# Optimization experiments

Measured on AMD Instinct MI355X. Metric: run time of the kernel, lower is better.

## Reference

```python
import jax, jax.numpy as jnp
import numpy as np

B, N, D = 4, 8192, 512
L, W, S = 64, 64, 32  # num_tokens, win_size, stride


def setup_inputs() -> dict:
    key = jax.random.key(0)
    ks = jax.random.split(key, 12)
    inp = {
        "feats": jax.random.normal(ks[0], (B, N, D), jnp.float32),
        "coords": jax.random.normal(ks[1], (B, N, 2), jnp.float32) * 100.0,
        "mask": jnp.zeros((B, N), dtype=bool),
        "z": jax.random.normal(ks[2], (L, D), jnp.float32) * 0.02,
        "Wq": jax.random.normal(ks[3], (D, D), jnp.float32) * 0.01,
        "Wk": jax.random.normal(ks[4], (D, D), jnp.float32) * 0.01,
        "Wv": jax.random.normal(ks[5], (D, D), jnp.float32) * 0.01,
        "W1": jax.random.normal(ks[6], (D, 2), jnp.float32) * 0.05,
        "b1": jnp.zeros((D,), jnp.float32),
        "W2": jax.random.normal(ks[7], (D, D), jnp.float32) * 0.01,
        "b2": jnp.zeros((D,), jnp.float32),
        "Wo": jax.random.normal(ks[8], (D, D), jnp.float32) * 0.01,
        "bo": jnp.zeros((D,), jnp.float32),
    }
    return inp


def reference(feats, coords, mask, z, Wq, Wk, Wv, W1, b1, W2, b2, Wo, bo):
    # mask is all-False: every token valid, N_valid == N, segments are
    # contiguous blocks of P = N // L tokens (seg_id = floor(i*L/N)).
    Bz, Nn, Dd = feats.shape
    Ll = z.shape[0]
    P = Nn // Ll  # tokens per segment

    # LayerNorm over feature dim (no affine, eps=1e-5 as in F.layer_norm)
    mu = feats.mean(-1, keepdims=True)
    var = feats.var(-1, keepdims=True)
    f_ln = (feats - mu) * jax.lax.rsqrt(var + 1e-5)

    # per-sample coordinate normalization (torch std is unbiased, ddof=1)
    c_mu = coords.mean(1, keepdims=True)
    c_sd = coords.std(1, keepdims=True, ddof=1) + 1e-8
    c_n = (coords - c_mu) / c_sd

    f_seg = f_ln.reshape(Bz, Ll, P, Dd)
    c_seg = c_n.reshape(Bz, Ll, P, 2)

    # static sliding windows within each segment (last window may be partial)
    starts = np.arange(0, P, S)                      # [nw]
    idx = starts[:, None] + np.arange(W)[None, :]    # [nw, W]
    valid = jnp.asarray(idx < P)                     # [nw, W] bool
    idx_c = np.minimum(idx, P - 1)
    cnt = valid.sum(-1).astype(feats.dtype)          # [nw]

    f_win = f_seg[:, :, idx_c]                       # [B,L,nw,W,D]
    c_win = c_seg[:, :, idx_c]                       # [B,L,nw,W,2]

    vmask = valid.astype(feats.dtype)[None, None, :, :, None]
    c_mean = (c_win * vmask).sum(3) / cnt[None, None, :, None]   # [B,L,nw,2]
    pos_in = c_win - c_mean[:, :, :, None, :]
    h = jax.nn.relu(jnp.einsum('blnwc,dc->blnwd', pos_in, W1) + b1)
    pos_bias = jnp.einsum('blnwd,ed->blnwe', h, W2) + b2

    q = z @ Wq.T                                     # [L,D]
    k = jnp.einsum('blnwd,ed->blnwe', f_win, Wk) + pos_bias
    v = jnp.einsum('blnwd,ed->blnwe', f_win, Wv)

    temperature = jnp.sqrt(jnp.asarray(Dd, feats.dtype))
    logits = jnp.einsum('ld,blnwd->blnw', q, k) / temperature
    logits = jnp.clip(logits, -10.0, 10.0)
    logits = jnp.where(valid[None, None], logits, -jnp.inf)
    attn = jax.nn.softmax(logits, axis=-1)           # [B,L,nw,W]

    z_win = jnp.einsum('blnw,blnwd->blnd', attn, v)  # [B,L,nw,D]
    z_l = z_win.mean(2)                              # average over windows
    return z_l @ Wo.T + bo                           # [B,L,D]
```

## Files before the change

kernel.cpp:

```cpp
#include <hip/hip_runtime.h>

#define Bz 4
#define Nn 8192
#define Dd 512
#define Ll 64
#define Pp 128
#define Ww 64
#define Ss 32
#define NW 4

__global__ __launch_bounds__(256) void pre1(
    const float* __restrict__ coords, const float* __restrict__ b2,
    const float* __restrict__ Wq, const float* __restrict__ Wk,
    const float* __restrict__ W2,
    const float* __restrict__ Wv, const float* __restrict__ Wo,
    float* __restrict__ cstats,
    float* __restrict__ M1, float* __restrict__ M2,
    float* __restrict__ WvoT, float* __restrict__ vb8) {
    __shared__ float As[64][68];
    __shared__ float Bs[64][68];
    __shared__ float b2s[64];
    __shared__ double dred[16];
    int bid = blockIdx.x, tid = threadIdx.x;
    int wv = tid >> 6, lane = tid & 63;

    if (bid < 192) {
        int role = bid >> 6;
        int wb = bid & 63;
        int m0 = (wb >> 3) * 64;
        int n0 = (wb & 7) * 64;
        const float* Amat = (role == 2) ? Wv : Wq;
        const float* Bmat = (role == 0) ? Wk : (role == 1) ? W2 : Wo;
        float* Cmat = (role == 0) ? M1 : (role == 1) ? M2 : WvoT;
        int tx = tid & 15, ty = tid >> 4;
        float4 acc[4];
#pragma unroll
        for (int i = 0; i < 4; ++i) acc[i] = make_float4(0.f, 0.f, 0.f, 0.f);

        for (int k0 = 0; k0 < Dd; k0 += 64) {
            {
                int kk = tid >> 4, q4 = (tid & 15) * 4;
#pragma unroll
                for (int i = 0; i < 4; ++i) {
                    int k = kk + 16 * i;
                    *(float4*)&As[k][q4] =
                        *(const float4*)&Amat[(size_t)(k0 + k) * Dd + m0 + q4];
                }
                if (role != 2) {
#pragma unroll
                    for (int i = 0; i < 4; ++i) {
                        int k = kk + 16 * i;
                        *(float4*)&Bs[k][q4] =
                            *(const float4*)&Bmat[(size_t)(k0 + k) * Dd + n0 + q4];
                    }
                } else {
                    int d = tid >> 2;
#pragma unroll
                    for (int j = 0; j < 4; ++j) {
                        int c0 = (tid & 3) * 16 + 4 * j;
                        float4 v = *(const float4*)&Bmat[(size_t)(n0 + d) * Dd + k0 + c0];
                        Bs[c0 + 0][d] = v.x; Bs[c0 + 1][d] = v.y;
                        Bs[c0 + 2][d] = v.z; Bs[c0 + 3][d] = v.w;
                    }
                }
            }
            __syncthreads();
#pragma unroll 8
            for (int kk = 0; kk < 64; ++kk) {
                float4 a4 = *(const float4*)&As[kk][ty * 4];
                float4 b4 = *(const float4*)&Bs[kk][tx * 4];
                acc[0].x = fmaf(a4.x, b4.x, acc[0].x); acc[0].y = fmaf(a4.x, b4.y, acc[0].y);
                acc[0].z = fmaf(a4.x, b4.z, acc[0].z); acc[0].w = fmaf(a4.x, b4.w, acc[0].w);
                acc[1].x = fmaf(a4.y, b4.x, acc[1].x); acc[1].y = fmaf(a4.y, b4.y, acc[1].y);
                acc[1].z = fmaf(a4.y, b4.z, acc[1].z); acc[1].w = fmaf(a4.y, b4.w, acc[1].w);
                acc[2].x = fmaf(a4.z, b4.x, acc[2].x); acc[2].y = fmaf(a4.z, b4.y, acc[2].y);
                acc[2].z = fmaf(a4.z, b4.z, acc[2].z); acc[2].w = fmaf(a4.z, b4.w, acc[2].w);
                acc[3].x = fmaf(a4.w, b4.x, acc[3].x); acc[3].y = fmaf(a4.w, b4.y, acc[3].y);
                acc[3].z = fmaf(a4.w, b4.z, acc[3].z); acc[3].w = fmaf(a4.w, b4.w, acc[3].w);
            }
            __syncthreads();
        }
#pragma unroll
        for (int i = 0; i < 4; ++i)
            *(float4*)&Cmat[(size_t)(m0 + ty * 4 + i) * Dd + n0 + tx * 4] = acc[i];
    } else if (bid < 200) {
        int j = bid - 192;
        if (tid < 64) b2s[tid] = b2[j * 64 + tid];
        __syncthreads();
        float a0 = 0.f, a1 = 0.f;
#pragma unroll 4
        for (int ee = 0; ee < 64; ++ee) {
            int e = j * 64 + ee;
            float be = b2s[ee];
            a0 = fmaf(be, Wq[(size_t)e * Dd + tid], a0);
            a1 = fmaf(be, Wq[(size_t)e * Dd + tid + 256], a1);
        }
        vb8[j * Dd + tid] = a0;
        vb8[j * Dd + tid + 256] = a1;
    } else {
        int b = bid - 200;
        double sx = 0, sy = 0, sxx = 0, syy = 0;
        const float4* cp = (const float4*)(coords + (size_t)b * Nn * 2);
        for (int i = tid; i < Nn / 2; i += 256) {
            float4 v = cp[i];
            sx  += (double)v.x + (double)v.z;
            sy  += (double)v.y + (double)v.w;
            sxx += (double)v.x * v.x + (double)v.z * v.z;
            syy += (double)v.y * v.y + (double)v.w * v.w;
        }
        for (int o = 32; o > 0; o >>= 1) {
            sx  += __shfl_down(sx,  o); sy  += __shfl_down(sy,  o);
            sxx += __shfl_down(sxx, o); syy += __shfl_down(syy, o);
        }
        if (lane == 0) {
            dred[wv * 4 + 0] = sx;  dred[wv * 4 + 1] = sy;
            dred[wv * 4 + 2] = sxx; dred[wv * 4 + 3] = syy;
        }
        __syncthreads();
        if (tid == 0) {
            double tx = 0, ty = 0, txx = 0, tyy = 0;
            for (int i = 0; i < 4; ++i) {
                tx += dred[i * 4 + 0]; ty += dred[i * 4 + 1];
                txx += dred[i * 4 + 2]; tyy += dred[i * 4 + 3];
            }
            const double N = (double)Nn;
            double mux = tx / N, muy = ty / N;
            double vx = (txx - N * mux * mux) / (N - 1.0);
            double vy = (tyy - N * muy * muy) / (N - 1.0);
            cstats[b * 4 + 0] = (float)mux;
            cstats[b * 4 + 1] = (float)muy;
            cstats[b * 4 + 2] = (float)sqrt(vx) + 1e-8f;
            cstats[b * 4 + 3] = (float)sqrt(vy) + 1e-8f;
        }
    }
}

__global__ __launch_bounds__(256) void qkg_k(
    const float* __restrict__ z, const float* __restrict__ M1,
    const float* __restrict__ M2, const float* __restrict__ vb8,
    float* __restrict__ QK, float* __restrict__ G,
    float* __restrict__ sqk4, float* __restrict__ qb2) {
    __shared__ float zs[Dd];
    __shared__ float pq[8][128];
    __shared__ float pg[8][128];
    __shared__ float red[8];
    int bid = blockIdx.x, tid = threadIdx.x;
    int l = bid & 63, ch = bid >> 6;
    int wv = tid >> 6, lane = tid & 63;

    zs[tid]       = z[(size_t)l * Dd + tid];
    zs[tid + 256] = z[(size_t)l * Dd + tid + 256];
    __syncthreads();

    if (ch == 0) {
        float vba = 0.f, vbb = 0.f;
#pragma unroll
        for (int j = 0; j < 8; ++j) {
            vba += vb8[j * Dd + tid];
            vbb += vb8[j * Dd + tid + 256];
        }
        float p = zs[tid] * vba + zs[tid + 256] * vbb;
        for (int o = 32; o > 0; o >>= 1) p += __shfl_xor(p, o);
        if (lane == 0) red[4 + wv] = p;
    }

    {
        int qd = tid & 31, h = tid >> 5;
        int cb = ch * 128 + qd * 4;
        float4 aq = make_float4(0.f, 0.f, 0.f, 0.f);
        float4 ag = make_float4(0.f, 0.f, 0.f, 0.f);
        for (int d = h * 64; d < h * 64 + 64; ++d) {
            float zd = zs[d];
            float4 m1 = *(const float4*)&M1[(size_t)d * Dd + cb];
            float4 m2 = *(const float4*)&M2[(size_t)d * Dd + cb];
            aq.x = fmaf(zd, m1.x, aq.x); aq.y = fmaf(zd, m1.y, aq.y);
            aq.z = fmaf(zd, m1.z, aq.z); aq.w = fmaf(zd, m1.w, aq.w);
            ag.x = fmaf(zd, m2.x, ag.x); ag.y = fmaf(zd, m2.y, ag.y);
            ag.z = fmaf(zd, m2.z, ag.z); ag.w = fmaf(zd, m2.w, ag.w);
        }
        *(float4*)&pq[h][qd * 4] = aq;
        *(float4*)&pg[h][qd * 4] = ag;
    }
    __syncthreads();
    if (tid < 128) {
        float vq = 0.f, vg = 0.f;
#pragma unroll
        for (int hh = 0; hh < 8; ++hh) { vq += pq[hh][tid]; vg += pg[hh][tid]; }
        QK[(size_t)l * Dd + ch * 128 + tid] = vq;
        G [(size_t)l * Dd + ch * 128 + tid] = vg;
        float s = vq;
        for (int o = 32; o > 0; o >>= 1) s += __shfl_xor(s, o);
        if (lane == 0) red[wv] = s;
    }
    __syncthreads();
    if (tid == 0) sqk4[ch * 64 + l] = red[0] + red[1];
    if (ch == 0 && tid == 32) qb2[l] = red[4] + red[5] + red[6] + red[7];
}

__global__ __launch_bounds__(1024) void attn2(
    const float* __restrict__ feats, const float* __restrict__ coords,
    const float* __restrict__ cstats,
    const float* __restrict__ QKm, const float* __restrict__ Gm,
    const float* __restrict__ sqk4, const float* __restrict__ qb2,
    const float* __restrict__ W1, const float* __restrict__ b1,
    const float* __restrict__ WvoT, const float* __restrict__ bo,
    float* __restrict__ out) {
    __shared__ float  qk_s[Dd];
    __shared__ float4 wpack[Dd];
    __shared__ float  scx[Pp], scy[Pp];
    __shared__ float  smu[Pp], srs[Pp], sa[Pp];
    __shared__ float  shs[NW * Ww];
    __shared__ float  sar[NW][Ww];
    __shared__ float  swt[Pp];
    __shared__ float  s2red[NW];
    __shared__ float  soff;
    __shared__ float  red16[16][Dd];

    int bx = blockIdx.x;
    int l = bx & 63, b = bx >> 6;
    int tid = threadIdx.x;
    int wv = tid >> 6, lane = tid & 63;

    if (tid < Dd) {
        qk_s[tid] = QKm[l * Dd + tid];
    } else {
        int t = tid - Dd;
        wpack[t] = make_float4(W1[2 * t], W1[2 * t + 1], b1[t], Gm[l * Dd + t]);
    }
    if (tid < Pp) {
        int row = bx * Pp + tid;
        float x = coords[(size_t)row * 2], y = coords[(size_t)row * 2 + 1];
        scx[tid] = (x - cstats[b * 4 + 0]) / cstats[b * 4 + 2];
        scy[tid] = (y - cstats[b * 4 + 1]) / cstats[b * 4 + 3];
    }
    float sqk_l = sqk4[l] + sqk4[64 + l] + sqk4[128 + l] + sqk4[192 + l];
    float qb2_l = qb2[l];
    __syncthreads();

    const float* fbase = feats + (size_t)bx * Pp * Dd;
    int rb = wv * 8;
    float4 f0[8], f1[8];
#pragma unroll
    for (int i = 0; i < 8; ++i) {
        const float4* fr = (const float4*)(fbase + (size_t)(rb + i) * Dd);
        f0[i] = fr[lane];
        f1[i] = fr[lane + 64];
    }
    __builtin_amdgcn_sched_barrier(0);

    float cmx[4], cmy[4];
#pragma unroll
    for (int n = 0; n < 4; ++n) {
        int nv = (n == 3) ? 32 : 64;
        float cx = (lane < nv) ? scx[n * Ss + lane] : 0.f;
        float cy = (lane < nv) ? scy[n * Ss + lane] : 0.f;
        for (int o = 32; o > 0; o >>= 1) { cx += __shfl_xor(cx, o); cy += __shfl_xor(cy, o); }
        cmx[n] = cx / (float)nv; cmy[n] = cy / (float)nv;
    }

    {
        int s = tid >> 2, q = tid & 3;
        int n = s >> 6, w = s & 63;
        int nv = (n == 3) ? 32 : 64;
        float hs = 0.f;
        if (w < nv) {
            int p = n * Ss + w;
            float px = scx[p] - cmx[n], py = scy[p] - cmy[n];
            int d0 = q * 128;
#pragma unroll 4
            for (int d = d0; d < d0 + 128; ++d) {
                float4 c = wpack[d];
                hs = fmaf(c.w, fmaxf(fmaf(c.x, px, fmaf(c.y, py, c.z)), 0.f), hs);
            }
        }
        hs += __shfl_xor(hs, 1);
        hs += __shfl_xor(hs, 2);
        if (q == 0) shs[s] = hs;
    }

    {
        float4 q0 = ((const float4*)qk_s)[lane];
        float4 q1 = ((const float4*)qk_s)[lane + 64];
#pragma unroll
        for (int b2i = 0; b2i < 8; b2i += 4) {
            float sP[4], ssP[4], aP[4];
#pragma unroll
            for (int i = 0; i < 4; ++i) {
                float4 v0 = f0[b2i + i], v1 = f1[b2i + i];
                sP[i]  = v0.x + v0.y + v0.z + v0.w + v1.x + v1.y + v1.z + v1.w;
                ssP[i] = v0.x * v0.x + v0.y * v0.y + v0.z * v0.z + v0.w * v0.w
                       + v1.x * v1.x + v1.y * v1.y + v1.z * v1.z + v1.w * v1.w;
                aP[i]  = v0.x * q0.x + v0.y * q0.y + v0.z * q0.z + v0.w * q0.w
                       + v1.x * q1.x + v1.y * q1.y + v1.z * q1.z + v1.w * q1.w;
            }
#pragma unroll
            for (int o = 32; o > 0; o >>= 1) {
#pragma unroll
                for (int i = 0; i < 4; ++i) {
                    sP[i] += __shfl_xor(sP[i], o); ssP[i] += __shfl_xor(ssP[i], o);
                    aP[i] += __shfl_xor(aP[i], o);
                }
            }
            if (lane == 0) {
#pragma unroll
                for (int i = 0; i < 4; ++i) {
                    int r = rb + b2i + i;
                    float mu  = sP[i] * (1.f / (float)Dd);
                    float var = ssP[i] * (1.f / (float)Dd) - mu * mu;
                    smu[r] = mu; srs[r] = 1.f / sqrtf(var + 1e-5f); sa[r] = aP[i];
                }
            }
        }
    }
    __syncthreads();

    const float invtemp = 0.04419417382415922f;
    if (wv < 4) {
        int n = wv, w = lane;
        int nv = (n == 3) ? 32 : 64;
        int p = n * Ss + ((w < nv) ? w : 0);
        float lg = -1e30f;
        if (w < nv) {
            lg = (srs[p] * (sa[p] - smu[p] * sqk_l) + shs[n * Ww + w] + qb2_l) * invtemp;
            lg = fminf(fmaxf(lg, -10.f), 10.f);
        }
        float m = lg;
        for (int o = 32; o > 0; o >>= 1) m = fmaxf(m, __shfl_xor(m, o));
        float e = (w < nv) ? expf(lg - m) : 0.f;
        float ssum = e;
        for (int o = 32; o > 0; o >>= 1) ssum += __shfl_xor(ssum, o);
        float ar = (w < nv) ? (e / ssum) * srs[p] : 0.f;
        sar[n][w] = ar;
        float t2 = (w < nv) ? ar * smu[p] : 0.f;
        for (int o = 32; o > 0; o >>= 1) t2 += __shfl_xor(t2, o);
        if (lane == 0) s2red[n] = t2;
    }
    __syncthreads();

    if (tid < Pp) {
        int p = tid;
        int na = (p >> 5) - 1, nb = (p >> 5);
        float wt = 0.f;
        if (na >= 0 && na <= 3) wt += sar[na][p - na * Ss];
        if (nb <= 3)            wt += sar[nb][p - nb * Ss];
        swt[p] = wt;
    }
    if (tid == 0) soff = 0.25f * (s2red[0] + s2red[1] + s2red[2] + s2red[3]);
    __syncthreads();

    {
        float4 a0 = make_float4(0.f, 0.f, 0.f, 0.f);
        float4 a1 = make_float4(0.f, 0.f, 0.f, 0.f);
#pragma unroll
        for (int i = 0; i < 8; ++i) {
            float wt = swt[rb + i];
            a0.x = fmaf(wt, f0[i].x, a0.x); a0.y = fmaf(wt, f0[i].y, a0.y);
            a0.z = fmaf(wt, f0[i].z, a0.z); a0.w = fmaf(wt, f0[i].w, a0.w);
            a1.x = fmaf(wt, f1[i].x, a1.x); a1.y = fmaf(wt, f1[i].y, a1.y);
            a1.z = fmaf(wt, f1[i].z, a1.z); a1.w = fmaf(wt, f1[i].w, a1.w);
        }
        *(float4*)&red16[wv][lane * 4]       = a0;
        *(float4*)&red16[wv][256 + lane * 4] = a1;
    }
    __syncthreads();
    if (tid < Dd) {
        float v = 0.f;
#pragma unroll
        for (int w = 0; w < 16; ++w) v += red16[w][tid];
        qk_s[tid] = 0.25f * v - soff;
    }
    __syncthreads();

    {
        int h = tid >> 7, cq = (tid & 127) * 4;
        float4 acc = make_float4(0.f, 0.f, 0.f, 0.f);
#pragma unroll 4
        for (int e = h * 64; e < h * 64 + 64; ++e) {
            float fe = qk_s[e];
            float4 w = *(const float4*)&WvoT[(size_t)e * Dd + cq];
            acc.x = fmaf(fe, w.x, acc.x);
            acc.y = fmaf(fe, w.y, acc.y);
            acc.z = fmaf(fe, w.z, acc.z);
            acc.w = fmaf(fe, w.w, acc.w);
        }
        *(float4*)&red16[h][cq] = acc;
    }
    __syncthreads();
    if (tid < Dd) {
        out[(size_t)bx * Dd + tid] = bo[tid]
            + red16[0][tid] + red16[1][tid] + red16[2][tid] + red16[3][tid]
            + red16[4][tid] + red16[5][tid] + red16[6][tid] + red16[7][tid];
    }
}

extern "C" void kernel_launch(void* const* d_in, const int* in_sizes, int n_in,
                              void* d_out, int out_size, void* d_ws, size_t ws_size,
                              hipStream_t stream) {
    const float* feats  = (const float*)d_in[0];
    const float* coords = (const float*)d_in[1];
    const float* z  = (const float*)d_in[3];
    const float* Wq = (const float*)d_in[4];
    const float* Wk = (const float*)d_in[5];
    const float* Wv = (const float*)d_in[6];
    const float* W1 = (const float*)d_in[7];
    const float* b1 = (const float*)d_in[8];
    const float* W2 = (const float*)d_in[9];
    const float* b2 = (const float*)d_in[10];
    const float* Wo = (const float*)d_in[11];
    const float* bo = (const float*)d_in[12];
    float* out = (float*)d_out;

    float* ws = (float*)d_ws;
    float* cstats = ws;
    float* M1     = ws + 16;
    float* M2     = M1 + Dd * Dd;
    float* WvoT   = M2 + Dd * Dd;
    float* vb8    = WvoT + Dd * Dd;
    float* QK     = vb8 + 8 * Dd;
    float* G      = QK + Ll * Dd;
    float* sqk4   = G + Ll * Dd;
    float* qb2    = sqk4 + 256;

    pre1<<<204, 256, 0, stream>>>(coords, b2, Wq, Wk, W2, Wv, Wo,
                                  cstats, M1, M2, WvoT, vb8);
    qkg_k<<<256, 256, 0, stream>>>(z, M1, M2, vb8, QK, G, sqk4, qb2);
    attn2<<<Bz * Ll, 1024, 0, stream>>>(feats, coords, cstats,
                                        QK, G, sqk4, qb2, W1, b1,
                                        WvoT, bo, out);
}
```

Measured before the change: 174.6 us.

## Fuse three kernels into one cooperative kernel with grid syncs

Replaces the three separate launches (weight-product precompute, per-token query projections, and attention/output) with a single cooperative kernel of 256 blocks by 1024 threads, separated by grid-wide syncs. The aim is to remove launch overhead and inter-kernel gaps between the small stages. In exchange, the first two stages now run on 1024-thread blocks in which only 256 threads are active, and grid.sync adds its own barrier cost.

```diff
diff --git a/kernel.cpp b/kernel.cpp
--- a/kernel.cpp
+++ b/kernel.cpp
@@ -1,4 +1,6 @@
 #include <hip/hip_runtime.h>
+#include <hip/hip_cooperative_groups.h>
+namespace cg = cooperative_groups;
 
 #define Bz 4
 #define Nn 8192
@@ -9,387 +11,396 @@
 #define Ss 32
 #define NW 4
 
-__global__ __launch_bounds__(256) void pre1(
-    const float* __restrict__ coords, const float* __restrict__ b2,
-    const float* __restrict__ Wq, const float* __restrict__ Wk,
-    const float* __restrict__ W2,
-    const float* __restrict__ Wv, const float* __restrict__ Wo,
-    float* __restrict__ cstats,
-    float* __restrict__ M1, float* __restrict__ M2,
-    float* __restrict__ WvoT, float* __restrict__ vb8) {
-    __shared__ float As[64][68];
-    __shared__ float Bs[64][68];
-    __shared__ float b2s[64];
-    __shared__ double dred[16];
+__global__ __launch_bounds__(1024) void fused(
+    const float* __restrict__ feats, const float* __restrict__ coords,
+    const float* __restrict__ z,  const float* __restrict__ Wq,
+    const float* __restrict__ Wk, const float* __restrict__ W2,
+    const float* __restrict__ b2, const float* __restrict__ Wv,
+    const float* __restrict__ Wo, const float* __restrict__ W1,
+    const float* __restrict__ b1, const float* __restrict__ bo,
+    float* cstats, float* M1, float* M2, float* WvoT, float* vb8,
+    float* QK, float* G, float* sqk4, float* qb2, float* out) {
+    cg::grid_group grid = cg::this_grid();
+    __shared__ __align__(16) char smem[48256];
     int bid = blockIdx.x, tid = threadIdx.x;
-    int wv = tid >> 6, lane = tid & 63;
-
-    if (bid < 192) {
-        int role = bid >> 6;
-        int wb = bid & 63;
-        int m0 = (wb >> 3) * 64;
-        int n0 = (wb & 7) * 64;
-        const float* Amat = (role == 2) ? Wv : Wq;
-        const float* Bmat = (role == 0) ? Wk : (role == 1) ? W2 : Wo;
-        float* Cmat = (role == 0) ? M1 : (role == 1) ? M2 : WvoT;
-        int tx = tid & 15, ty = tid >> 4;
-        float4 acc[4];
-#pragma unroll
-        for (int i = 0; i < 4; ++i) acc[i] = make_float4(0.f, 0.f, 0.f, 0.f);
-
-        for (int k0 = 0; k0 < Dd; k0 += 64) {
-            {
-                int kk = tid >> 4, q4 = (tid & 15) * 4;
-#pragma unroll
-                for (int i = 0; i < 4; ++i) {
-                    int k = kk + 16 * i;
-                    *(float4*)&As[k][q4] =
-                        *(const float4*)&Amat[(size_t)(k0 + k) * Dd + m0 + q4];
-                }
-                if (role != 2) {
+
+    {
+        bool act = (tid < 256);
+        int wv4 = tid >> 6, lane = tid & 63;
+        if (bid < 192) {
+            float (*As)[68] = (float (*)[68])smem;
+            float (*Bs)[68] = (float (*)[68])(smem + 17408);
+            int role = bid >> 6;
+            int wb = bid & 63;
+            int m0 = (wb >> 3) * 64;
+            int n0 = (wb & 7) * 64;
+            const float* Amat = (role == 2) ? Wv : Wq;
+            const float* Bmat = (role == 0) ? Wk : (role == 1) ? W2 : Wo;
+            float* Cmat = (role == 0) ? M1 : (role == 1) ? M2 : WvoT;
+            int tx = tid & 15, ty = (tid & 255) >> 4;
+            float4 acc[4];
+#pragma unroll
+            for (int i = 0; i < 4; ++i) acc[i] = make_float4(0.f, 0.f, 0.f, 0.f);
+
+            for (int k0 = 0; k0 < Dd; k0 += 64) {
+                if (act) {
+                    int kk = tid >> 4, q4 = (tid & 15) * 4;
 #pragma unroll
                     for (int i = 0; i < 4; ++i) {
                         int k = kk + 16 * i;
-                        *(float4*)&Bs[k][q4] =
-                            *(const float4*)&Bmat[(size_t)(k0 + k) * Dd + n0 + q4];
+                        *(float4*)&As[k][q4] =
+                            *(const float4*)&Amat[(size_t)(k0 + k) * Dd + m0 + q4];
                     }
-                } else {
-                    int d = tid >> 2;
-#pragma unroll
-                    for (int j = 0; j < 4; ++j) {
-                        int c0 = (tid & 3) * 16 + 4 * j;
-                        float4 v = *(const float4*)&Bmat[(size_t)(n0 + d) * Dd + k0 + c0];
-                        Bs[c0 + 0][d] = v.x; Bs[c0 + 1][d] = v.y;
-                        Bs[c0 + 2][d] = v.z; Bs[c0 + 3][d] = v.w;
+                    if (role != 2) {
+#pragma unroll
+                        for (int i = 0; i < 4; ++i) {
+                            int k = kk + 16 * i;
+                            *(float4*)&Bs[k][q4] =
+                                *(const float4*)&Bmat[(size_t)(k0 + k) * Dd + n0 + q4];
+                        }
+                    } else {
+                        int d = tid >> 2;
+#pragma unroll
+                        for (int j = 0; j < 4; ++j) {
+                            int c0 = (tid & 3) * 16 + 4 * j;
+                            float4 v = *(const float4*)&Bmat[(size_t)(n0 + d) * Dd + k0 + c0];
+                            Bs[c0 + 0][d] = v.x; Bs[c0 + 1][d] = v.y;
+                            Bs[c0 + 2][d] = v.z; Bs[c0 + 3][d] = v.w;
+                        }
                     }
                 }
-            }
+                __syncthreads();
+                if (act) {
+#pragma unroll 8
+                    for (int kk = 0; kk < 64; ++kk) {
+                        float4 a4 = *(const float4*)&As[kk][ty * 4];
+                        float4 b4 = *(const float4*)&Bs[kk][tx * 4];
+                        acc[0].x = fmaf(a4.x, b4.x, acc[0].x); acc[0].y = fmaf(a4.x, b4.y, acc[0].y);
+                        acc[0].z = fmaf(a4.x, b4.z, acc[0].z); acc[0].w = fmaf(a4.x, b4.w, acc[0].w);
+                        acc[1].x = fmaf(a4.y, b4.x, acc[1].x); acc[1].y = fmaf(a4.y, b4.y, acc[1].y);
+                        acc[1].z = fmaf(a4.y, b4.z, acc[1].z); acc[1].w = fmaf(a4.y, b4.w, acc[1].w);
+                        acc[2].x = fmaf(a4.z, b4.x, acc[2].x); acc[2].y = fmaf(a4.z, b4.y, acc[2].y);
+                        acc[2].z = fmaf(a4.z, b4.z, acc[2].z); acc[2].w = fmaf(a4.z, b4.w, acc[2].w);
+                        acc[3].x = fmaf(a4.w, b4.x, acc[3].x); acc[3].y = fmaf(a4.w, b4.y, acc[3].y);
+                        acc[3].z = fmaf(a4.w, b4.z, acc[3].z); acc[3].w = fmaf(a4.w, b4.w, acc[3].w);
+                    }
+                }
+                __syncthreads();
+            }
+            if (act) {
+#pragma unroll
+                for (int i = 0; i < 4; ++i)
+                    *(float4*)&Cmat[(size_t)(m0 + ty * 4 + i) * Dd + n0 + tx * 4] = acc[i];
+            }
+        } else if (bid < 200) {
+            float* b2s = (float*)(smem + 34816);
+            int j = bid - 192;
+            if (act && tid < 64) b2s[tid] = b2[j * 64 + tid];
             __syncthreads();
-#pragma unroll 8
-            for (int kk = 0; kk < 64; ++kk) {
-                float4 a4 = *(const float4*)&As[kk][ty * 4];
-                float4 b4 = *(const float4*)&Bs[kk][tx * 4];
-                acc[0].x = fmaf(a4.x, b4.x, acc[0].x); acc[0].y = fmaf(a4.x, b4.y, acc[0].y);
-                acc[0].z = fmaf(a4.x, b4.z, acc[0].z); acc[0].w = fmaf(a4.x, b4.w, acc[0].w);
-                acc[1].x = fmaf(a4.y, b4.x, acc[1].x); acc[1].y = fmaf(a4.y, b4.y, acc[1].y);
-                acc[1].z = fmaf(a4.y, b4.z, acc[1].z); acc[1].w = fmaf(a4.y, b4.w, acc[1].w);
-                acc[2].x = fmaf(a4.z, b4.x, acc[2].x); acc[2].y = fmaf(a4.z, b4.y, acc[2].y);
-                acc[2].z = fmaf(a4.z, b4.z, acc[2].z); acc[2].w = fmaf(a4.z, b4.w, acc[2].w);
-                acc[3].x = fmaf(a4.w, b4.x, acc[3].x); acc[3].y = fmaf(a4.w, b4.y, acc[3].y);
-                acc[3].z = fmaf(a4.w, b4.z, acc[3].z); acc[3].w = fmaf(a4.w, b4.w, acc[3].w);
+            if (act) {
+                float a0 = 0.f, a1 = 0.f;
+#pragma unroll 4
+                for (int ee = 0; ee < 64; ++ee) {
+                    int e = j * 64 + ee;
+                    float be = b2s[ee];
+                    a0 = fmaf(be, Wq[(size_t)e * Dd + tid], a0);
+                    a1 = fmaf(be, Wq[(size_t)e * Dd + tid + 256], a1);
+                }
+                vb8[j * Dd + tid] = a0;
+                vb8[j * Dd + tid + 256] = a1;
+            }
+        } else if (bid < 204) {
+            double* dred = (double*)(smem + 35072);
+            int b = bid - 200;
+            if (act) {
+                double sx = 0, sy = 0, sxx = 0, syy = 0;
+                const float4* cp = (const float4*)(coords + (size_t)b * Nn * 2);
+                for (int i = tid; i < Nn / 2; i += 256) {
+                    float4 v = cp[i];
+                    sx  += (double)v.x + (double)v.z;
+                    sy  += (double)v.y + (double)v.w;
+                    sxx += (double)v.x * v.x + (double)v.z * v.z;
+                    syy += (double)v.y * v.y + (double)v.w * v.w;
+                }
+                for (int o = 32; o > 0; o >>= 1) {
+                    sx  += __shfl_down(sx,  o); sy  += __shfl_down(sy,  o);
+                    sxx += __shfl_down(sxx, o); syy += __shfl_down(syy, o);
+                }
+                if (lane == 0) {
+                    dred[wv4 * 4 + 0] = sx;  dred[wv4 * 4 + 1] = sy;
+                    dred[wv4 * 4 + 2] = sxx; dred[wv4 * 4 + 3] = syy;
+                }
             }
             __syncthreads();
-        }
-#pragma unroll
-        for (int i = 0; i < 4; ++i)
-            *(float4*)&Cmat[(size_t)(m0 + ty * 4 + i) * Dd + n0 + tx * 4] = acc[i];
-    } else if (bid < 200) {
-        int j = bid - 192;
-        if (tid < 64) b2s[tid] = b2[j * 64 + tid];
-        __syncthreads();
-        float a0 = 0.f, a1 = 0.f;
+            if (tid == 0) {
+                double tx = 0, ty = 0, txx = 0, tyy = 0;
+                for (int i = 0; i < 4; ++i) {
+                    tx += dred[i * 4 + 0]; ty += dred[i * 4 + 1];
+                    txx += dred[i * 4 + 2]; tyy += dred[i * 4 + 3];
+                }
+                const double N = (double)Nn;
+                double mux = tx / N, muy = ty / N;
+                double vx = (txx - N * mux * mux) / (N - 1.0);
+                double vy = (tyy - N * muy * muy) / (N - 1.0);
+                cstats[b * 4 + 0] = (float)mux;
+                cstats[b * 4 + 1] = (float)muy;
+                cstats[b * 4 + 2] = (float)sqrt(vx) + 1e-8f;
+                cstats[b * 4 + 3] = (float)sqrt(vy) + 1e-8f;
+            }
+        }
+    }
+    __threadfence();
+    grid.sync();
+
+    {
+        float* zs        = (float*)smem;
+        float (*pq)[128] = (float (*)[128])(smem + 2048);
+        float (*pg)[128] = (float (*)[128])(smem + 6144);
+        float* redB      = (float*)(smem + 10240);
+        bool act = (tid < 256);
+        int l = bid & 63, ch = bid >> 6;
+        int wv4 = tid >> 6, lane = tid & 63;
+
+        if (act) {
+            zs[tid]       = z[(size_t)l * Dd + tid];
+            zs[tid + 256] = z[(size_t)l * Dd + tid + 256];
+        }
+        __syncthreads();
+        if (act) {
+            if (ch == 0) {
+                float vba = 0.f, vbb = 0.f;
+#pragma unroll
+                for (int j = 0; j < 8; ++j) {
+                    vba += vb8[j * Dd + tid];
+                    vbb += vb8[j * Dd + tid + 256];
+                }
+                float p = zs[tid] * vba + zs[tid + 256] * vbb;
+                for (int o = 32; o > 0; o >>= 1) p += __shfl_xor(p, o);
+                if (lane == 0) redB[4 + wv4] = p;
+            }
+            int qd = tid & 31, h = tid >> 5;
+            int cb = ch * 128 + qd * 4;
+            float4 aq = make_float4(0.f, 0.f, 0.f, 0.f);
+            float4 ag = make_float4(0.f, 0.f, 0.f, 0.f);
+            for (int d = h * 64; d < h * 64 + 64; ++d) {
+                float zd = zs[d];
+                float4 m1 = *(const float4*)&M1[(size_t)d * Dd + cb];
+                float4 m2 = *(const float4*)&M2[(size_t)d * Dd + cb];
+                aq.x = fmaf(zd, m1.x, aq.x); aq.y = fmaf(zd, m1.y, aq.y);
+                aq.z = fmaf(zd, m1.z, aq.z); aq.w = fmaf(zd, m1.w, aq.w);
+                ag.x = fmaf(zd, m2.x, ag.x); ag.y = fmaf(zd, m2.y, ag.y);
+                ag.z = fmaf(zd, m2.z, ag.z); ag.w = fmaf(zd, m2.w, ag.w);
+            }
+            *(float4*)&pq[h][qd * 4] = aq;
+            *(float4*)&pg[h][qd * 4] = ag;
+        }
+        __syncthreads();
+        if (act && tid < 128) {
+            float vq = 0.f, vg = 0.f;
+#pragma unroll
+            for (int hh = 0; hh < 8; ++hh) { vq += pq[hh][tid]; vg += pg[hh][tid]; }
+            QK[(size_t)l * Dd + ch * 128 + tid] = vq;
+            G [(size_t)l * Dd + ch * 128 + tid] = vg;
+            float s = vq;
+            for (int o = 32; o > 0; o >>= 1) s += __shfl_xor(s, o);
+            if (lane == 0) redB[wv4] = s;
+        }
+        __syncthreads();
+        if (tid == 0) sqk4[ch * 64 + l] = redB[0] + redB[1];
+        if (ch == 0 && tid == 32) qb2[l] = redB[4] + redB[5] + redB[6] + redB[7];
+    }
+    __threadfence();
+    grid.sync();
+
+    {
+        float*  qk_s  = (float*)smem;
+        float4* wpack = (float4*)(smem + 2048);
+        float*  scx   = (float*)(smem + 10240);
+        float*  scy   = (float*)(smem + 10752);
+        float*  smu   = (float*)(smem + 11264);
+        float*  srs   = (float*)(smem + 11776);
+        float*  sa    = (float*)(smem + 12288);
+        float*  shs   = (float*)(smem + 12800);
+        float (*sar)[Ww] = (float (*)[Ww])(smem + 13824);
+        float*  swt   = (float*)(smem + 14848);
+        float*  s2red = (float*)(smem + 15360);
+        float*  soff  = (float*)(smem + 15376);
+        float (*red16)[Dd] = (float (*)[Dd])(smem + 15392);
+
+        int bx = bid;
+        int l = bx & 63, b = bx >> 6;
+        int wv = tid >> 6, lane = tid & 63;
+
+        if (tid < Dd) {
+            qk_s[tid] = QK[l * Dd + tid];
+        } else {
+            int t = tid - Dd;
+            wpack[t] = make_float4(W1[2 * t], W1[2 * t + 1], b1[t], G[l * Dd + t]);
+        }
+        if (tid < Pp) {
+            int row = bx * Pp + tid;
+            float x = coords[(size_t)row * 2], y = coords[(size_t)row * 2 + 1];
+            scx[tid] = (x - cstats[b * 4 + 0]) / cstats[b * 4 + 2];
+            scy[tid] = (y - cstats[b * 4 + 1]) / cstats[b * 4 + 3];
+        }
+        float sqk_l = sqk4[l] + sqk4[64 + l] + sqk4[128 + l] + sqk4[192 + l];
+        float qb2_l = qb2[l];
+        __syncthreads();
+
+        const float* fbase = feats + (size_t)bx * Pp * Dd;
+        int rb = wv * 8;
+        float4 f0[8], f1[8];
+#pragma unroll
+        for (int i = 0; i < 8; ++i) {
+            const float4* fr = (const float4*)(fbase + (size_t)(rb + i) * Dd);
+            f0[i] = fr[lane];
+            f1[i] = fr[lane + 64];
+        }
+        __builtin_amdgcn_sched_barrier(0);
+
+        float cmx[4], cmy[4];
+#pragma unroll
+        for (int n = 0; n < 4; ++n) {
+            int nv = (n == 3) ? 32 : 64;
+            float cx = (lane < nv) ? scx[n * Ss + lane] : 0.f;
+            float cy = (lane < nv) ? scy[n * Ss + lane] : 0.f;
+            for (int o = 32; o > 0; o >>= 1) { cx += __shfl_xor(cx, o); cy += __shfl_xor(cy, o); }
+            cmx[n] = cx / (float)nv; cmy[n] = cy / (float)nv;
+        }
+
+        {
+            int s = tid >> 2, q = tid & 3;
+            int n = s >> 6, w = s & 63;
+            int nv = (n == 3) ? 32 : 64;
+            float hs = 0.f;
+            if (w < nv) {
+                int p = n * Ss + w;
+                float px = scx[p] - cmx[n], py = scy[p] - cmy[n];
+                int d0 = q * 128;
 #pragma unroll 4
-        for (int ee = 0; ee < 64; ++ee) {
-            int e = j * 64 + ee;
-            float be = b2s[ee];
-            a0 = fmaf(be, Wq[(size_t)e * Dd + tid], a0);
-            a1 = fmaf(be, Wq[(size_t)e * Dd + tid + 256], a1);
-        }
-        vb8[j * Dd + tid] = a0;
-        vb8[j * Dd + tid + 256] = a1;
-    } else {
-        int b = bid - 200;
-        double sx = 0, sy = 0, sxx = 0, syy = 0;
-        const float4* cp = (const float4*)(coords + (size_t)b * Nn * 2);
-        for (int i = tid; i < Nn / 2; i += 256) {
-            float4 v = cp[i];
-            sx  += (double)v.x + (double)v.z;
-            sy  += (double)v.y + (double)v.w;
-            sxx += (double)v.x * v.x + (double)v.z * v.z;
-            syy += (double)v.y * v.y + (double)v.w * v.w;
-        }
-        for (int o = 32; o > 0; o >>= 1) {
-            sx  += __shfl_down(sx,  o); sy  += __shfl_down(sy,  o);
-            sxx += __shfl_down(sxx, o); syy += __shfl_down(syy, o);
-        }
-        if (lane == 0) {
-            dred[wv * 4 + 0] = sx;  dred[wv * 4 + 1] = sy;
-            dred[wv * 4 + 2] = sxx; dred[wv * 4 + 3] = syy;
-        }
-        __syncthreads();
-        if (tid == 0) {
-            double tx = 0, ty = 0, txx = 0, tyy = 0;
-            for (int i = 0; i < 4; ++i) {
-                tx += dred[i * 4 + 0]; ty += dred[i * 4 + 1];
-                txx += dred[i * 4 + 2]; tyy += dred[i * 4 + 3];
-            }
-            const double N = (double)Nn;
-            double mux = tx / N, muy = ty / N;
-            double vx = (txx - N * mux * mux) / (N - 1.0);
-            double vy = (tyy - N * muy * muy) / (N - 1.0);
-            cstats[b * 4 + 0] = (float)mux;
-            cstats[b * 4 + 1] = (float)muy;
-            cstats[b * 4 + 2] = (float)sqrt(vx) + 1e-8f;
-            cstats[b * 4 + 3] = (float)sqrt(vy) + 1e-8f;
-        }
-    }
-}
-
-__global__ __launch_bounds__(256) void qkg_k(
-    const float* __restrict__ z, const float* __restrict__ M1,
-    const float* __restrict__ M2, const float* __restrict__ vb8,
-    float* __restrict__ QK, float* __restrict__ G,
-    float* __restrict__ sqk4, float* __restrict__ qb2) {
-    __shared__ float zs[Dd];
-    __shared__ float pq[8][128];
-    __shared__ float pg[8][128];
-    __shared__ float red[8];
-    int bid = blockIdx.x, tid = threadIdx.x;
-    int l = bid & 63, ch = bid >> 6;
-    int wv = tid >> 6, lane = tid & 63;
-
-    zs[tid]       = z[(size_t)l * Dd + tid];
-    zs[tid + 256] = z[(size_t)l * Dd + tid + 256];
-    __syncthreads();
-
-    if (ch == 0) {
-        float vba = 0.f, vbb = 0.f;
-#pragma unroll
-        for (int j = 0; j < 8; ++j) {
-            vba += vb8[j * Dd + tid];
-            vbb += vb8[j * Dd + tid + 256];
-        }
-        float p = zs[tid] * vba + zs[tid + 256] * vbb;
-        for (int o = 32; o > 0; o >>= 1) p += __shfl_xor(p, o);
-        if (lane == 0) red[4 + wv] = p;
-    }
-
-    {
-        int qd = tid & 31, h = tid >> 5;
-        int cb = ch * 128 + qd * 4;
-        float4 aq = make_float4(0.f, 0.f, 0.f, 0.f);
-        float4 ag = make_float4(0.f, 0.f, 0.f, 0.f);
-        for (int d = h * 64; d < h * 64 + 64; ++d) {
-            float zd = zs[d];
-            float4 m1 = *(const float4*)&M1[(size_t)d * Dd + cb];
-            float4 m2 = *(const float4*)&M2[(size_t)d * Dd + cb];
-            aq.x = fmaf(zd, m1.x, aq.x); aq.y = fmaf(zd, m1.y, aq.y);
-            aq.z = fmaf(zd, m1.z, aq.z); aq.w = fmaf(zd, m1.w, aq.w);
-            ag.x = fmaf(zd, m2.x, ag.x); ag.y = fmaf(zd, m2.y, ag.y);
-            ag.z = fmaf(zd, m2.z, ag.z); ag.w = fmaf(zd, m2.w, ag.w);
-        }
-        *(float4*)&pq[h][qd * 4] = aq;
-        *(float4*)&pg[h][qd * 4] = ag;
-    }
-    __syncthreads();
-    if (tid < 128) {
-        float vq = 0.f, vg = 0.f;
-#pragma unroll
-        for (int hh = 0; hh < 8; ++hh) { vq += pq[hh][tid]; vg += pg[hh][tid]; }
-        QK[(size_t)l * Dd + ch * 128 + tid] = vq;
-        G [(size_t)l * Dd + ch * 128 + tid] = vg;
-        float s = vq;
-        for (int o = 32; o > 0; o >>= 1) s += __shfl_xor(s, o);
-        if (lane == 0) red[wv] = s;
-    }
-    __syncthreads();
-    if (tid == 0) sqk4[ch * 64 + l] = red[0] + red[1];
-    if (ch == 0 && tid == 32) qb2[l] = red[4] + red[5] + red[6] + red[7];
-}
-
-__global__ __launch_bounds__(1024) void attn2(
-    const float* __restrict__ feats, const float* __restrict__ coords,
-    const float* __restrict__ cstats,
-    const float* __restrict__ QKm, const float* __restrict__ Gm,
-    const float* __restrict__ sqk4, const float* __restrict__ qb2,
-    const float* __restrict__ W1, const float* __restrict__ b1,
-    const float* __restrict__ WvoT, const float* __restrict__ bo,
-    float* __restrict__ out) {
-    __shared__ float  qk_s[Dd];
-    __shared__ float4 wpack[Dd];
-    __shared__ float  scx[Pp], scy[Pp];
-    __shared__ float  smu[Pp], srs[Pp], sa[Pp];
-    __shared__ float  shs[NW * Ww];
-    __shared__ float  sar[NW][Ww];
-    __shared__ float  swt[Pp];
-    __shared__ float  s2red[NW];
-    __shared__ float  soff;
-    __shared__ float  red16[16][Dd];
-
-    int bx = blockIdx.x;
-    int l = bx & 63, b = bx >> 6;
-    int tid = threadIdx.x;
-    int wv = tid >> 6, lane = tid & 63;
-
-    if (tid < Dd) {
-        qk_s[tid] = QKm[l * Dd + tid];
-    } else {
-        int t = tid - Dd;
-        wpack[t] = make_float4(W1[2 * t], W1[2 * t + 1], b1[t], Gm[l * Dd + t]);
-    }
-    if (tid < Pp) {
-        int row = bx * Pp + tid;
-        float x = coords[(size_t)row * 2], y = coords[(size_t)row * 2 + 1];
-        scx[tid] = (x - cstats[b * 4 + 0]) / cstats[b * 4 + 2];
-        scy[tid] = (y - cstats[b * 4 + 1]) / cstats[b * 4 + 3];
-    }
-    float sqk_l = sqk4[l] + sqk4[64 + l] + sqk4[128 + l] + sqk4[192 + l];
-    float qb2_l = qb2[l];
-    __syncthreads();
-
-    const float* fbase = feats + (size_t)bx * Pp * Dd;
-    int rb = wv * 8;
-    float4 f0[8], f1[8];
-#pragma unroll
-    for (int i = 0; i < 8; ++i) {
-        const float4* fr = (const float4*)(fbase + (size_t)(rb + i) * Dd);
-        f0[i] = fr[lane];
-        f1[i] = fr[lane + 64];
-    }
-    __builtin_amdgcn_sched_barrier(0);
-
-    float cmx[4], cmy[4];
-#pragma unroll
-    for (int n = 0; n < 4; ++n) {
-        int nv = (n == 3) ? 32 : 64;
-        float cx = (lane < nv) ? scx[n * Ss + lane] : 0.f;
-        float cy = (lane < nv) ? scy[n * Ss + lane] : 0.f;
-        for (int o = 32; o > 0; o >>= 1) { cx += __shfl_xor(cx, o); cy += __shfl_xor(cy, o); }
-        cmx[n] = cx / (float)nv; cmy[n] = cy / (float)nv;
-    }
-
-    {
-        int s = tid >> 2, q = tid & 3;
-        int n = s >> 6, w = s & 63;
-        int nv = (n == 3) ? 32 : 64;
-        float hs = 0.f;
-        if (w < nv) {
-            int p = n * Ss + w;
-            float px = scx[p] - cmx[n], py = scy[p] - cmy[n];
-            int d0 = q * 128;
+                for (int d = d0; d < d0 + 128; ++d) {
+                    float4 c = wpack[d];
+                    hs = fmaf(c.w, fmaxf(fmaf(c.x, px, fmaf(c.y, py, c.z)), 0.f), hs);
+                }
+            }
+            hs += __shfl_xor(hs, 1);
+            hs += __shfl_xor(hs, 2);
+            if (q == 0) shs[s] = hs;
+        }
+
+        {
+            float4 q0 = ((const float4*)qk_s)[lane];
+            float4 q1 = ((const float4*)qk_s)[lane + 64];
+#pragma unroll
+            for (int b2i = 0; b2i < 8; b2i += 4) {
+                float sP[4], ssP[4], aP[4];
+#pragma unroll
+                for (int i = 0; i < 4; ++i) {
+                    float4 v0 = f0[b2i + i], v1 = f1[b2i + i];
+                    sP[i]  = v0.x + v0.y + v0.z + v0.w + v1.x + v1.y + v1.z + v1.w;
+                    ssP[i] = v0.x * v0.x + v0.y * v0.y + v0.z * v0.z + v0.w * v0.w
+                           + v1.x * v1.x + v1.y * v1.y + v1.z * v1.z + v1.w * v1.w;
+                    aP[i]  = v0.x * q0.x + v0.y * q0.y + v0.z * q0.z + v0.w * q0.w
+                           + v1.x * q1.x + v1.y * q1.y + v1.z * q1.z + v1.w * q1.w;
+                }
+#pragma unroll
+                for (int o = 32; o > 0; o >>= 1) {
+#pragma unroll
+                    for (int i = 0; i < 4; ++i) {
+                        sP[i] += __shfl_xor(sP[i], o); ssP[i] += __shfl_xor(ssP[i], o);
+                        aP[i] += __shfl_xor(aP[i], o);
+                    }
+                }
+                if (lane == 0) {
+#pragma unroll
+                    for (int i = 0; i < 4; ++i) {
+                        int r = rb + b2i + i;
+                        float mu  = sP[i] * (1.f / (float)Dd);
+                        float var = ssP[i] * (1.f / (float)Dd) - mu * mu;
+                        smu[r] = mu; srs[r] = 1.f / sqrtf(var + 1e-5f); sa[r] = aP[i];
+                    }
+                }
+            }
+        }
+        __syncthreads();
+
+        const float invtemp = 0.04419417382415922f;
+        if (wv < 4) {
+            int n = wv, w = lane;
+            int nv = (n == 3) ? 32 : 64;
+            int p = n * Ss + ((w < nv) ? w : 0);
+            float lg = -1e30f;
+            if (w < nv) {
+                lg = (srs[p] * (sa[p] - smu[p] * sqk_l) + shs[n * Ww + w] + qb2_l) * invtemp;
+                lg = fminf(fmaxf(lg, -10.f), 10.f);
+            }
+            float m = lg;
+            for (int o = 32; o > 0; o >>= 1) m = fmaxf(m, __shfl_xor(m, o));
+            float e = (w < nv) ? expf(lg - m) : 0.f;
+            float ssum = e;
+            for (int o = 32; o > 0; o >>= 1) ssum += __shfl_xor(ssum, o);
+            float ar = (w < nv) ? (e / ssum) * srs[p] : 0.f;
+            sar[n][w] = ar;
+            float t2 = (w < nv) ? ar * smu[p] : 0.f;
+            for (int o = 32; o > 0; o >>= 1) t2 += __shfl_xor(t2, o);
+            if (lane == 0) s2red[n] = t2;
+        }
+        __syncthreads();
+
+        if (tid < Pp) {
+            int p = tid;
+            int na = (p >> 5) - 1, nb = (p >> 5);
+            float wt = 0.f;
+            if (na >= 0 && na <= 3) wt += sar[na][p - na * Ss];
+            if (nb <= 3)            wt += sar[nb][p - nb * Ss];
+            swt[p] = wt;
+        }
+        if (tid == 0) *soff = 0.25f * (s2red[0] + s2red[1] + s2red[2] + s2red[3]);
+        __syncthreads();
+
+        {
+            float4 a0 = make_float4(0.f, 0.f, 0.f, 0.f);
+            float4 a1 = make_float4(0.f, 0.f, 0.f, 0.f);
+#pragma unroll
+            for (int i = 0; i < 8; ++i) {
+                float wt = swt[rb + i];
+                a0.x = fmaf(wt, f0[i].x, a0.x); a0.y = fmaf(wt, f0[i].y, a0.y);
+                a0.z = fmaf(wt, f0[i].z, a0.z); a0.w = fmaf(wt, f0[i].w, a0.w);
+                a1.x = fmaf(wt, f1[i].x, a1.x); a1.y = fmaf(wt, f1[i].y, a1.y);
+                a1.z = fmaf(wt, f1[i].z, a1.z); a1.w = fmaf(wt, f1[i].w, a1.w);
+            }
+            *(float4*)&red16[wv][lane * 4]       = a0;
+            *(float4*)&red16[wv][256 + lane * 4] = a1;
+        }
+        __syncthreads();
+        if (tid < Dd) {
+            float v = 0.f;
+#pragma unroll
+            for (int w = 0; w < 16; ++w) v += red16[w][tid];
+            qk_s[tid] = 0.25f * v - *soff;
+        }
+        __syncthreads();
+
+        {
+            int h = tid >> 7, cq = (tid & 127) * 4;
+            float4 acc = make_float4(0.f, 0.f, 0.f, 0.f);
 #pragma unroll 4
-            for (int d = d0; d < d0 + 128; ++d) {
-                float4 c = wpack[d];
-                hs = fmaf(c.w, fmaxf(fmaf(c.x, px, fmaf(c.y, py, c.z)), 0.f), hs);
-            }
-        }
-        hs += __shfl_xor(hs, 1);
-        hs += __shfl_xor(hs, 2);
-        if (q == 0) shs[s] = hs;
-    }
-
-    {
-        float4 q0 = ((const float4*)qk_s)[lane];
-        float4 q1 = ((const float4*)qk_s)[lane + 64];
-#pragma unroll
-        for (int b2i = 0; b2i < 8; b2i += 4) {
-            float sP[4], ssP[4], aP[4];
-#pragma unroll
-            for (int i = 0; i < 4; ++i) {
-                float4 v0 = f0[b2i + i], v1 = f1[b2i + i];
-                sP[i]  = v0.x + v0.y + v0.z + v0.w + v1.x + v1.y + v1.z + v1.w;
-                ssP[i] = v0.x * v0.x + v0.y * v0.y + v0.z * v0.z + v0.w * v0.w
-                       + v1.x * v1.x + v1.y * v1.y + v1.z * v1.z + v1.w * v1.w;
-                aP[i]  = v0.x * q0.x + v0.y * q0.y + v0.z * q0.z + v0.w * q0.w
-                       + v1.x * q1.x + v1.y * q1.y + v1.z * q1.z + v1.w * q1.w;
-            }
-#pragma unroll
-            for (int o = 32; o > 0; o >>= 1) {
-#pragma unroll
-                for (int i = 0; i < 4; ++i) {
-                    sP[i] += __shfl_xor(sP[i], o); ssP[i] += __shfl_xor(ssP[i], o);
-                    aP[i] += __shfl_xor(aP[i], o);
-                }
-            }
-            if (lane == 0) {
-#pragma unroll
-                for (int i = 0; i < 4; ++i) {
-                    int r = rb + b2i + i;
-                    float mu  = sP[i] * (1.f / (float)Dd);
-                    float var = ssP[i] * (1.f / (float)Dd) - mu * mu;
-                    smu[r] = mu; srs[r] = 1.f / sqrtf(var + 1e-5f); sa[r] = aP[i];
-                }
-            }
-        }
-    }
-    __syncthreads();
-
-    const float invtemp = 0.04419417382415922f;
-    if (wv < 4) {
-        int n = wv, w = lane;
-        int nv = (n == 3) ? 32 : 64;
-        int p = n * Ss + ((w < nv) ? w : 0);
-        float lg = -1e30f;
-        if (w < nv) {
-            lg = (srs[p] * (sa[p] - smu[p] * sqk_l) + shs[n * Ww + w] + qb2_l) * invtemp;
-            lg = fminf(fmaxf(lg, -10.f), 10.f);
-        }
-        float m = lg;
-        for (int o = 32; o > 0; o >>= 1) m = fmaxf(m, __shfl_xor(m, o));
-        float e = (w < nv) ? expf(lg - m) : 0.f;
-        float ssum = e;
-        for (int o = 32; o > 0; o >>= 1) ssum += __shfl_xor(ssum, o);
-        float ar = (w < nv) ? (e / ssum) * srs[p] : 0.f;
-        sar[n][w] = ar;
-        float t2 = (w < nv) ? ar * smu[p] : 0.f;
-        for (int o = 32; o > 0; o >>= 1) t2 += __shfl_xor(t2, o);
-        if (lane == 0) s2red[n] = t2;
-    }
-    __syncthreads();
-
-    if (tid < Pp) {
-        int p = tid;
-        int na = (p >> 5) - 1, nb = (p >> 5);
-        float wt = 0.f;
-        if (na >= 0 && na <= 3) wt += sar[na][p - na * Ss];
-        if (nb <= 3)            wt += sar[nb][p - nb * Ss];
-        swt[p] = wt;
-    }
-    if (tid == 0) soff = 0.25f * (s2red[0] + s2red[1] + s2red[2] + s2red[3]);
-    __syncthreads();
-
-    {
-        float4 a0 = make_float4(0.f, 0.f, 0.f, 0.f);
-        float4 a1 = make_float4(0.f, 0.f, 0.f, 0.f);
-#pragma unroll
-        for (int i = 0; i < 8; ++i) {
-            float wt = swt[rb + i];
-            a0.x = fmaf(wt, f0[i].x, a0.x); a0.y = fmaf(wt, f0[i].y, a0.y);
-            a0.z = fmaf(wt, f0[i].z, a0.z); a0.w = fmaf(wt, f0[i].w, a0.w);
-            a1.x = fmaf(wt, f1[i].x, a1.x); a1.y = fmaf(wt, f1[i].y, a1.y);
-            a1.z = fmaf(wt, f1[i].z, a1.z); a1.w = fmaf(wt, f1[i].w, a1.w);
-        }
-        *(float4*)&red16[wv][lane * 4]       = a0;
-        *(float4*)&red16[wv][256 + lane * 4] = a1;
-    }
-    __syncthreads();
-    if (tid < Dd) {
-        float v = 0.f;
-#pragma unroll
-        for (int w = 0; w < 16; ++w) v += red16[w][tid];
-        qk_s[tid] = 0.25f * v - soff;
-    }
-    __syncthreads();
-
-    {
-        int h = tid >> 7, cq = (tid & 127) * 4;
-        float4 acc = make_float4(0.f, 0.f, 0.f, 0.f);
-#pragma unroll 4
-        for (int e = h * 64; e < h * 64 + 64; ++e) {
-            float fe = qk_s[e];
-            float4 w = *(const float4*)&WvoT[(size_t)e * Dd + cq];
-            acc.x = fmaf(fe, w.x, acc.x);
-            acc.y = fmaf(fe, w.y, acc.y);
-            acc.z = fmaf(fe, w.z, acc.z);
-            acc.w = fmaf(fe, w.w, acc.w);
-        }
-        *(float4*)&red16[h][cq] = acc;
-    }
-    __syncthreads();
-    if (tid < Dd) {
-        out[(size_t)bx * Dd + tid] = bo[tid]
-            + red16[0][tid] + red16[1][tid] + red16[2][tid] + red16[3][tid]
-            + red16[4][tid] + red16[5][tid] + red16[6][tid] + red16[7][tid];
+            for (int e = h * 64; e < h * 64 + 64; ++e) {
+                float fe = qk_s[e];
+                float4 w = *(const float4*)&WvoT[(size_t)e * Dd + cq];
+                acc.x = fmaf(fe, w.x, acc.x);
+                acc.y = fmaf(fe, w.y, acc.y);
+                acc.z = fmaf(fe, w.z, acc.z);
+                acc.w = fmaf(fe, w.w, acc.w);
+            }
+            *(float4*)&red16[h][cq] = acc;
+        }
+        __syncthreads();
+        if (tid < Dd) {
+            out[(size_t)bx * Dd + tid] = bo[tid]
+                + red16[0][tid] + red16[1][tid] + red16[2][tid] + red16[3][tid]
+                + red16[4][tid] + red16[5][tid] + red16[6][tid] + red16[7][tid];
+        }
     }
 }
 
@@ -421,10 +432,13 @@
     float* sqk4   = G + Ll * Dd;
     float* qb2    = sqk4 + 256;
 
-    pre1<<<204, 256, 0, stream>>>(coords, b2, Wq, Wk, W2, Wv, Wo,
-                                  cstats, M1, M2, WvoT, vb8);
-    qkg_k<<<256, 256, 0, stream>>>(z, M1, M2, vb8, QK, G, sqk4, qb2);
-    attn2<<<Bz * Ll, 1024, 0, stream>>>(feats, coords, cstats,
-                                        QK, G, sqk4, qb2, W1, b1,
-                                        WvoT, bo, out);
+    void* args[] = {
+        (void*)&feats, (void*)&coords, (void*)&z, (void*)&Wq, (void*)&Wk,
+        (void*)&W2, (void*)&b2, (void*)&Wv, (void*)&Wo, (void*)&W1,
+        (void*)&b1, (void*)&bo,
+        (void*)&cstats, (void*)&M1, (void*)&M2, (void*)&WvoT, (void*)&vb8,
+        (void*)&QK, (void*)&G, (void*)&sqk4, (void*)&qb2, (void*)&out
+    };
+    hipLaunchCooperativeKernel((const void*)fused, dim3(256), dim3(1024),
+                               args, 0, stream);
 }
```

Measured after the change: 387.3 us. +121.8%, slower.

## Fuse query-key projection kernel into attention kernel, dropping a launch

Applied to the files above, without the earlier changes.

Removes the separate qkg_k kernel and computes the per-token QK and G vectors, plus their scalar reductions, inside the attention kernel. The red16 shared buffer is reused for the partial sums. This saves one kernel launch and the global round trip for the intermediate vectors. The cost is that each of the 256 attention blocks now repeats the z·M1 and z·M2 products (4x redundancy across batch) and reads 2 MB of M1/M2, with an extra block-wide barrier.

```diff
diff --git a/kernel.cpp b/kernel.cpp
--- a/kernel.cpp
+++ b/kernel.cpp
@@ -135,77 +135,17 @@
     }
 }
 
-__global__ __launch_bounds__(256) void qkg_k(
-    const float* __restrict__ z, const float* __restrict__ M1,
-    const float* __restrict__ M2, const float* __restrict__ vb8,
-    float* __restrict__ QK, float* __restrict__ G,
-    float* __restrict__ sqk4, float* __restrict__ qb2) {
-    __shared__ float zs[Dd];
-    __shared__ float pq[8][128];
-    __shared__ float pg[8][128];
-    __shared__ float red[8];
-    int bid = blockIdx.x, tid = threadIdx.x;
-    int l = bid & 63, ch = bid >> 6;
-    int wv = tid >> 6, lane = tid & 63;
-
-    zs[tid]       = z[(size_t)l * Dd + tid];
-    zs[tid + 256] = z[(size_t)l * Dd + tid + 256];
-    __syncthreads();
-
-    if (ch == 0) {
-        float vba = 0.f, vbb = 0.f;
-#pragma unroll
-        for (int j = 0; j < 8; ++j) {
-            vba += vb8[j * Dd + tid];
-            vbb += vb8[j * Dd + tid + 256];
-        }
-        float p = zs[tid] * vba + zs[tid + 256] * vbb;
-        for (int o = 32; o > 0; o >>= 1) p += __shfl_xor(p, o);
-        if (lane == 0) red[4 + wv] = p;
-    }
-
-    {
-        int qd = tid & 31, h = tid >> 5;
-        int cb = ch * 128 + qd * 4;
-        float4 aq = make_float4(0.f, 0.f, 0.f, 0.f);
-        float4 ag = make_float4(0.f, 0.f, 0.f, 0.f);
-        for (int d = h * 64; d < h * 64 + 64; ++d) {
-            float zd = zs[d];
-            float4 m1 = *(const float4*)&M1[(size_t)d * Dd + cb];
-            float4 m2 = *(const float4*)&M2[(size_t)d * Dd + cb];
-            aq.x = fmaf(zd, m1.x, aq.x); aq.y = fmaf(zd, m1.y, aq.y);
-            aq.z = fmaf(zd, m1.z, aq.z); aq.w = fmaf(zd, m1.w, aq.w);
-            ag.x = fmaf(zd, m2.x, ag.x); ag.y = fmaf(zd, m2.y, ag.y);
-            ag.z = fmaf(zd, m2.z, ag.z); ag.w = fmaf(zd, m2.w, ag.w);
-        }
-        *(float4*)&pq[h][qd * 4] = aq;
-        *(float4*)&pg[h][qd * 4] = ag;
-    }
-    __syncthreads();
-    if (tid < 128) {
-        float vq = 0.f, vg = 0.f;
-#pragma unroll
-        for (int hh = 0; hh < 8; ++hh) { vq += pq[hh][tid]; vg += pg[hh][tid]; }
-        QK[(size_t)l * Dd + ch * 128 + tid] = vq;
-        G [(size_t)l * Dd + ch * 128 + tid] = vg;
-        float s = vq;
-        for (int o = 32; o > 0; o >>= 1) s += __shfl_xor(s, o);
-        if (lane == 0) red[wv] = s;
-    }
-    __syncthreads();
-    if (tid == 0) sqk4[ch * 64 + l] = red[0] + red[1];
-    if (ch == 0 && tid == 32) qb2[l] = red[4] + red[5] + red[6] + red[7];
-}
-
-__global__ __launch_bounds__(1024) void attn2(
+__global__ __launch_bounds__(1024) void attn3(
     const float* __restrict__ feats, const float* __restrict__ coords,
     const float* __restrict__ cstats,
-    const float* __restrict__ QKm, const float* __restrict__ Gm,
-    const float* __restrict__ sqk4, const float* __restrict__ qb2,
+    const float* __restrict__ M1, const float* __restrict__ M2,
+    const float* __restrict__ vb8, const float* __restrict__ z,
     const float* __restrict__ W1, const float* __restrict__ b1,
     const float* __restrict__ WvoT, const float* __restrict__ bo,
     float* __restrict__ out) {
     __shared__ float  qk_s[Dd];
+    __shared__ float  gw[Dd];
+    __shared__ float  zs[Dd];
     __shared__ float4 wpack[Dd];
     __shared__ float  scx[Pp], scy[Pp];
     __shared__ float  smu[Pp], srs[Pp], sa[Pp];
@@ -214,6 +154,7 @@
     __shared__ float  swt[Pp];
     __shared__ float  s2red[NW];
     __shared__ float  soff;
+    __shared__ float  redsc[16];
     __shared__ float  red16[16][Dd];
 
     int bx = blockIdx.x;
@@ -222,10 +163,13 @@
     int wv = tid >> 6, lane = tid & 63;
 
     if (tid < Dd) {
-        qk_s[tid] = QKm[l * Dd + tid];
+        zs[tid] = z[(size_t)l * Dd + tid];
     } else {
         int t = tid - Dd;
-        wpack[t] = make_float4(W1[2 * t], W1[2 * t + 1], b1[t], Gm[l * Dd + t]);
+        float vb = 0.f;
+#pragma unroll
+        for (int j = 0; j < 8; ++j) vb += vb8[j * Dd + t];
+        wpack[t] = make_float4(W1[2 * t], W1[2 * t + 1], b1[t], vb);
     }
     if (tid < Pp) {
         int row = bx * Pp + tid;
@@ -233,8 +177,6 @@
         scx[tid] = (x - cstats[b * 4 + 0]) / cstats[b * 4 + 2];
         scy[tid] = (y - cstats[b * 4 + 1]) / cstats[b * 4 + 3];
     }
-    float sqk_l = sqk4[l] + sqk4[64 + l] + sqk4[128 + l] + sqk4[192 + l];
-    float qb2_l = qb2[l];
     __syncthreads();
 
     const float* fbase = feats + (size_t)bx * Pp * Dd;
@@ -247,6 +189,23 @@
         f1[i] = fr[lane + 64];
     }
     __builtin_amdgcn_sched_barrier(0);
+
+    {
+        int h = tid >> 7, c4 = (tid & 127) * 4;
+        float4 aq = make_float4(0.f, 0.f, 0.f, 0.f);
+        float4 ag = make_float4(0.f, 0.f, 0.f, 0.f);
+        for (int d = h * 64; d < h * 64 + 64; ++d) {
+            float zd = zs[d];
+            float4 m1 = *(const float4*)&M1[(size_t)d * Dd + c4];
+            float4 m2 = *(const float4*)&M2[(size_t)d * Dd + c4];
+            aq.x = fmaf(zd, m1.x, aq.x); aq.y = fmaf(zd, m1.y, aq.y);
+            aq.z = fmaf(zd, m1.z, aq.z); aq.w = fmaf(zd, m1.w, aq.w);
+            ag.x = fmaf(zd, m2.x, ag.x); ag.y = fmaf(zd, m2.y, ag.y);
+            ag.z = fmaf(zd, m2.z, ag.z); ag.w = fmaf(zd, m2.w, ag.w);
+        }
+        *(float4*)&red16[h][c4]     = aq;
+        *(float4*)&red16[8 + h][c4] = ag;
+    }
 
     float cmx[4], cmy[4];
 #pragma unroll
@@ -257,6 +216,23 @@
         for (int o = 32; o > 0; o >>= 1) { cx += __shfl_xor(cx, o); cy += __shfl_xor(cy, o); }
         cmx[n] = cx / (float)nv; cmy[n] = cy / (float)nv;
     }
+    __syncthreads();
+
+    if (tid < Dd) {
+        float vq = 0.f, vg = 0.f;
+#pragma unroll
+        for (int h = 0; h < 8; ++h) { vq += red16[h][tid]; vg += red16[8 + h][tid]; }
+        qk_s[tid] = vq; gw[tid] = vg;
+        float pq = vq;
+        float pb = zs[tid] * wpack[tid].w;
+        for (int o = 32; o > 0; o >>= 1) { pq += __shfl_xor(pq, o); pb += __shfl_xor(pb, o); }
+        if (lane == 0) { redsc[wv] = pq; redsc[8 + wv] = pb; }
+    }
+    __syncthreads();
+    float sqk_l = redsc[0] + redsc[1] + redsc[2] + redsc[3]
+                + redsc[4] + redsc[5] + redsc[6] + redsc[7];
+    float qb2_l = redsc[8] + redsc[9] + redsc[10] + redsc[11]
+                + redsc[12] + redsc[13] + redsc[14] + redsc[15];
 
     {
         int s = tid >> 2, q = tid & 3;
@@ -270,7 +246,7 @@
 #pragma unroll 4
             for (int d = d0; d < d0 + 128; ++d) {
                 float4 c = wpack[d];
-                hs = fmaf(c.w, fmaxf(fmaf(c.x, px, fmaf(c.y, py, c.z)), 0.f), hs);
+                hs = fmaf(gw[d], fmaxf(fmaf(c.x, px, fmaf(c.y, py, c.z)), 0.f), hs);
             }
         }
         hs += __shfl_xor(hs, 1);
@@ -416,15 +392,10 @@
     float* M2     = M1 + Dd * Dd;
     float* WvoT   = M2 + Dd * Dd;
     float* vb8    = WvoT + Dd * Dd;
-    float* QK     = vb8 + 8 * Dd;
-    float* G      = QK + Ll * Dd;
-    float* sqk4   = G + Ll * Dd;
-    float* qb2    = sqk4 + 256;
 
     pre1<<<204, 256, 0, stream>>>(coords, b2, Wq, Wk, W2, Wv, Wo,
                                   cstats, M1, M2, WvoT, vb8);
-    qkg_k<<<256, 256, 0, stream>>>(z, M1, M2, vb8, QK, G, sqk4, qb2);
-    attn2<<<Bz * Ll, 1024, 0, stream>>>(feats, coords, cstats,
-                                        QK, G, sqk4, qb2, W1, b1,
+    attn3<<<Bz * Ll, 1024, 0, stream>>>(feats, coords, cstats,
+                                        M1, M2, vb8, z, W1, b1,
                                         WvoT, bo, out);
 }
```

Measured after the change: 211.2 us. 20.9% more time.
